# Performance work log

Hardware: AMD Instinct MI355X
Metric: run time of the kernel (lower is better)

## Reference

```python
import jax, jax.numpy as jnp
import numpy as np

N, E, H, L, R, NG = 8192, 131072, 256, 3, 128, 64
NUM_ELEMENTS = 80
CUTOFF = 12.0
INV_SQRT_2 = 1.0 / np.sqrt(2.0)
INV_SQRT_3 = 1.0 / np.sqrt(3.0)
INV_SQRT_H = 1.0 / np.sqrt(H)


def _glorot(key, shape):
    fan_in, fan_out = shape[-2], shape[-1]
    return jax.random.normal(key, shape, jnp.float32) * np.sqrt(2.0 / (fan_in + fan_out))


def setup_inputs():
    key = jax.random.key(0)
    ks = jax.random.split(key, 24)
    pos = jax.random.normal(ks[0], (N, 3), jnp.float32) * 5.0
    z = jax.random.randint(ks[1], (N,), 0, NUM_ELEMENTS)
    src = jax.random.randint(ks[2], (E,), 0, N)
    off = jax.random.randint(ks[3], (E,), 1, N)
    dst = (src + off) % N  # guarantee no self-loops (dist > 0)
    edge_index = jnp.stack([src, dst])
    batch = jnp.sort(jax.random.randint(ks[4], (N,), 0, NG))
    return {
        "pos": pos,
        "atom_emb": jax.random.normal(ks[5], (NUM_ELEMENTS, H), jnp.float32),
        "ln_w": jnp.ones((L, H), jnp.float32),
        "ln_b": jnp.zeros((L, H), jnp.float32),
        "xp_w1": _glorot(ks[6], (L, H, H)),
        "xp_b1": jnp.zeros((L, H), jnp.float32),
        "xp_w2": _glorot(ks[7], (L, H, 3 * H)),
        "xp_b2": jnp.zeros((L, 3 * H), jnp.float32),
        "rbf_w": _glorot(ks[8], (L, R, 3 * H)),
        "rbf_b": jnp.zeros((L, 3 * H), jnp.float32),
        "vec_w": _glorot(ks[9], (L, H, 2 * H)),
        "xv_w1": _glorot(ks[10], (L, 2 * H, H)),
        "xv_b1": jnp.zeros((L, H), jnp.float32),
        "xv_w2": _glorot(ks[11], (L, H, 3 * H)),
        "xv_b2": jnp.zeros((L, 3 * H), jnp.float32),
        "oe_w1": _glorot(ks[12], (H, H // 2)),
        "oe_b1": jnp.zeros((H // 2,), jnp.float32),
        "oe_w2": _glorot(ks[13], (H // 2, 1)),
        "oe_b2": jnp.zeros((1,), jnp.float32),
        "z": z,
        "edge_index": edge_index,
        "batch": batch,
    }


def _gaussian_rbf(dist):
    offset = jnp.linspace(0.0, CUTOFF, R)
    coeff = -0.5 / (offset[1] - offset[0]) ** 2
    return jnp.exp(coeff * (dist[:, None] - offset[None, :]) ** 2)  # [E, R]


def _layernorm(x, w, b):
    mu = x.mean(-1, keepdims=True)
    var = x.var(-1, keepdims=True)
    return (x - mu) / jnp.sqrt(var + 1e-5) * w + b


def reference(pos, atom_emb, ln_w, ln_b, xp_w1, xp_b1, xp_w2, xp_b2,
              rbf_w, rbf_b, vec_w, xv_w1, xv_b1, xv_w2, xv_b2,
              oe_w1, oe_b1, oe_w2, oe_b2, z, edge_index, batch):
    src, dst = edge_index[0], edge_index[1]
    rel = pos[src] - pos[dst]                       # [E, 3]
    dist = jnp.sqrt((rel ** 2).sum(-1))             # [E]
    edge_rbf = _gaussian_rbf(dist)                  # [E, R]
    edge_vector = rel / dist[:, None]               # [E, 3] unit vectors

    x = atom_emb[z]                                 # [N, H]
    vec = jnp.zeros((N, 3, H), x.dtype)

    for l in range(L):
        # ---- PaiNNMessage ----
        xh = _layernorm(x, ln_w[l], ln_b[l])
        xh = jax.nn.silu(xh @ xp_w1[l] + xp_b1[l]) @ xp_w2[l] + xp_b2[l]  # [N, 3H]
        rbfh = edge_rbf @ rbf_w[l] + rbf_b[l]                             # [E, 3H]
        m = xh[src] * rbfh
        mx, xh2, xh3 = jnp.split(m, 3, axis=-1)
        xh2 = xh2 * INV_SQRT_3
        mvec = (vec[src] * xh2[:, None, :] + xh3[:, None, :] * edge_vector[:, :, None]) * INV_SQRT_H
        dx = jax.ops.segment_sum(mx, dst, num_segments=N)
        dvec = jax.ops.segment_sum(mvec, dst, num_segments=N)
        x = (x + dx) * INV_SQRT_2
        vec = vec + dvec

        # ---- PaiNNUpdate ----
        vp = vec @ vec_w[l]                          # [N, 3, 2H]
        vec1, vec2 = jnp.split(vp, 2, axis=-1)
        vec_dot = (vec1 * vec2).sum(axis=1) * INV_SQRT_H           # [N, H]
        vnorm = jnp.sqrt((vec2 ** 2).sum(axis=1) + 1e-8)           # [N, H]
        h = jnp.concatenate([x, vnorm], axis=-1)
        h = jax.nn.silu(h @ xv_w1[l] + xv_b1[l]) @ xv_w2[l] + xv_b2[l]
        xv1, xv2, xv3 = jnp.split(h, 3, axis=-1)
        dx = (xv1 + xv2 * vec_dot) * INV_SQRT_2
        dvec = xv3[:, None, :] * vec1
        x = (x + dx) * INV_SQRT_2
        vec = vec + dvec

    # ---- energy head: per-atom MLP then per-molecule sum ----
    per_atom = jax.nn.silu(x @ oe_w1 + oe_b1) @ oe_w2 + oe_b2      # [N, 1]
    energy = jax.ops.segment_sum(per_atom, batch, num_segments=NG)  # [NG, 1]
    return energy
```

## Files before the change

### kernel.cpp

```cpp
#include <hip/hip_runtime.h>
#include <hip/hip_bf16.h>
#include <math.h>

#define NN 8192
#define EE 131072
#define HH 256
#define LL 3
#define RR 128
#define NGG 64
#define MSG_WAVES 16

typedef __attribute__((ext_vector_type(8))) short bf16x8;
typedef __attribute__((ext_vector_type(4))) float f32x4;
typedef unsigned short u16;

#if defined(__has_builtin)
#if __has_builtin(__builtin_amdgcn_fdot2_f32_bf16)
#define HAVE_FDOT2 1
typedef __attribute__((ext_vector_type(2))) __bf16 bf16x2_t;
union BU { unsigned u; bf16x2_t v; };
#endif
#if __has_builtin(__builtin_amdgcn_global_load_lds)
#define HAVE_GLL 1
#endif
#endif

union U4 { ushort4 v; unsigned short a[4]; };
union U8 { uint4 v; unsigned short a[8]; unsigned w[4]; };

__device__ __forceinline__ float silu(float v) { return v / (1.0f + expf(-v)); }
__device__ __forceinline__ float b2f(unsigned short u) { return __uint_as_float(((unsigned)u) << 16); }
__device__ __forceinline__ unsigned short f2b(float f) {
    unsigned u = __float_as_uint(f);
    u += 0x7fff + ((u >> 16) & 1);
    return (unsigned short)(u >> 16);
}

constexpr float kInvSqrt2 = 0.70710678118654752440f;
constexpr float kInvSqrt3 = 0.57735026918962576451f;
constexpr float kInvSqrtH = 0.0625f;

__global__ void k_zero(float* __restrict__ p, int n4) {
    int i = blockIdx.x * 256 + threadIdx.x;
    if (i < n4) ((float4*)p)[i] = make_float4(0.f, 0.f, 0.f, 0.f);
}

__global__ __launch_bounds__(256) void k_wt_all(
    const float* __restrict__ xp_w1, const float* __restrict__ xp_w2,
    const float* __restrict__ rbf_w, const float* __restrict__ vec_w,
    const float* __restrict__ xv_w1, const float* __restrict__ xv_w2,
    const float* __restrict__ oe_w1,
    u16* __restrict__ xp_w1T, u16* __restrict__ xp_w2T, u16* __restrict__ rbf_wP,
    u16* __restrict__ vec_wT, u16* __restrict__ xv_w1T, u16* __restrict__ xv_w2T,
    u16* __restrict__ oe_w1T) {
    int bid = blockIdx.x;
    const float* src; u16* dst; int K, N, t, pairmode = 0;
    if (bid < 2400) {
        int l = bid / 800, r = bid % 800;
        if (r < 64)       { src = xp_w1 + (size_t)l * 65536;  dst = xp_w1T + (size_t)l * 65536;  K = 256; N = 256; t = r; }
        else if (r < 256) { src = xp_w2 + (size_t)l * 196608; dst = xp_w2T + (size_t)l * 196608; K = 256; N = 768; t = r - 64; }
        else if (r < 352) { src = rbf_w + (size_t)l * 98304;  dst = rbf_wP + (size_t)l * 98304;  K = 128; N = 768; t = r - 256; pairmode = 1; }
        else if (r < 480) { src = vec_w + (size_t)l * 131072; dst = vec_wT + (size_t)l * 131072; K = 256; N = 512; t = r - 352; }
        else if (r < 608) { src = xv_w1 + (size_t)l * 131072; dst = xv_w1T + (size_t)l * 131072; K = 512; N = 256; t = r - 480; }
        else              { src = xv_w2 + (size_t)l * 196608; dst = xv_w2T + (size_t)l * 196608; K = 256; N = 768; t = r - 608; }
    } else {
        src = oe_w1; dst = oe_w1T; K = 256; N = 128; t = bid - 2400;
    }
    int nx = N >> 5;
    int bn = (t % nx) * 32, bk = (t / nx) * 32;
    int tx = threadIdx.x & 31, ty = threadIdx.x >> 5;
    if (pairmode) {
#pragma unroll
        for (int i = 0; i < 32; i += 8) {
            int k = bk + ty + i, n = bn + tx;
            dst[(size_t)(k >> 1) * 1536 + n * 2 + (k & 1)] = f2b(src[(size_t)k * N + n]);
        }
        return;
    }
    __shared__ float tile[32][33];
#pragma unroll
    for (int i = 0; i < 32; i += 8)
        tile[ty + i][tx] = src[(size_t)(bk + ty + i) * N + bn + tx];
    __syncthreads();
#pragma unroll
    for (int i = 0; i < 32; i += 8)
        dst[(size_t)(bn + ty + i) * K + bk + tx] = f2b(tile[tx][ty + i]);
}

__global__ void k_init_ln(const float* __restrict__ emb, const int* __restrict__ z,
                          const float* __restrict__ w, const float* __restrict__ b,
                          float* __restrict__ x, u16* __restrict__ xlnb) {
    int n = blockIdx.x, t = threadIdx.x;
    float v = emb[z[n] * HH + t];
    x[(size_t)n * HH + t] = v;
    float s = v, q = v * v;
#pragma unroll
    for (int m = 32; m >= 1; m >>= 1) {
        s += __shfl_xor(s, m, 64);
        q += __shfl_xor(q, m, 64);
    }
    __shared__ float s_sum[4], s_sq[4];
    int wid = t >> 6;
    if ((t & 63) == 0) { s_sum[wid] = s; s_sq[wid] = q; }
    __syncthreads();
    float S = s_sum[0] + s_sum[1] + s_sum[2] + s_sum[3];
    float Q = s_sq[0] + s_sq[1] + s_sq[2] + s_sq[3];
    float mu = S * (1.0f / HH);
    float var = Q * (1.0f / HH) - mu * mu;
    float rs = rsqrtf(var + 1e-5f);
    xlnb[(size_t)n * HH + t] = f2b((v - mu) * rs * w[t] + b[t]);
}

__global__ void k_geom_hist(const float* __restrict__ pos, const int* __restrict__ ei,
                            float* __restrict__ ev, int* __restrict__ deg) {
    int e = blockIdx.x * 256 + threadIdx.x;
    if (e >= EE) return;
    int s = ei[e], d = ei[EE + e];
    float rx = pos[s * 3 + 0] - pos[d * 3 + 0];
    float ry = pos[s * 3 + 1] - pos[d * 3 + 1];
    float rz = pos[s * 3 + 2] - pos[d * 3 + 2];
    float dist = sqrtf(rx * rx + ry * ry + rz * rz);
    float inv = 1.0f / dist;
    ((float4*)ev)[e] = make_float4(rx * inv, ry * inv, rz * inv, dist);
    atomicAdd(&deg[d], 1);
}

__global__ void k_scan_sort(const int* __restrict__ deg, int* __restrict__ row_ptr,
                            int* __restrict__ fill, int* __restrict__ dorder) {
    __shared__ int buf[256];
    __shared__ int carry_s;
    int t = threadIdx.x;
    if (t == 0) carry_s = 0;
    __syncthreads();
    for (int r = 0; r < NN; r += 256) {
        int v = deg[r + t];
        buf[t] = v;
        __syncthreads();
        for (int ofs = 1; ofs < 256; ofs <<= 1) {
            int add = (t >= ofs) ? buf[t - ofs] : 0;
            __syncthreads();
            buf[t] += add;
            __syncthreads();
        }
        int excl = buf[t] - v;
        int carry = carry_s;
        row_ptr[r + t] = carry + excl;
        fill[r + t] = carry + excl;
        __syncthreads();
        if (t == 255) carry_s = carry + buf[t];
        __syncthreads();
    }
    if (t == 0) row_ptr[NN] = carry_s;
    __syncthreads();
    __shared__ int bins[256];
    __shared__ int base[256];
    bins[t] = 0;
    __syncthreads();
    for (int d = t; d < NN; d += 256) {
        int b = deg[d]; b = b > 255 ? 255 : b;
        atomicAdd(&bins[b], 1);
    }
    __syncthreads();
    if (t == 0) {
        int acc = 0;
        for (int k = 255; k >= 0; --k) { base[k] = acc; acc += bins[k]; }
    }
    __syncthreads();
    bins[t] = 0;
    __syncthreads();
    for (int d = t; d < NN; d += 256) {
        int b = deg[d]; b = b > 255 ? 255 : b;
        int p = atomicAdd(&bins[b], 1);
        dorder[base[b] + p] = d;
    }
}

__global__ void k_scatter(const int* __restrict__ ei, const float* __restrict__ ev,
                          int* __restrict__ fill, int* __restrict__ srcp,
                          float4* __restrict__ evp, int* __restrict__ kptab,
                          unsigned* __restrict__ gtab) {
    int e = blockIdx.x * 256 + threadIdx.x;
    if (e >= EE) return;
    int d = ei[EE + e];
    int pos = atomicAdd(&fill[d], 1);
    float4 e4 = ((const float4*)ev)[e];
    srcp[pos] = ei[e];
    evp[pos] = e4;
    const float step = 12.0f / 127.0f;
    const float coeff = -0.5f / (step * step);
    float dist = e4.w;
    int k0 = ((int)floorf(dist / step) - 3) & ~1;
    k0 = k0 < 0 ? 0 : (k0 > 120 ? 120 : k0);
    float g[8];
#pragma unroll
    for (int k = 0; k < 8; ++k) {
        float t = dist - (k0 + k) * step;
        g[k] = expf(coeff * t * t);
    }
    kptab[pos] = k0 >> 1;
    unsigned g0 = (unsigned)f2b(g[0]) | ((unsigned)f2b(g[1]) << 16);
    unsigned g1 = (unsigned)f2b(g[2]) | ((unsigned)f2b(g[3]) << 16);
    unsigned g2 = (unsigned)f2b(g[4]) | ((unsigned)f2b(g[5]) << 16);
    unsigned g3 = (unsigned)f2b(g[6]) | ((unsigned)f2b(g[7]) << 16);
    ((uint4*)gtab)[pos] = make_uint4(g0, g1, g2, g3);
}

template <int OUT_BF16, int ACT>
__global__ __launch_bounds__(256) void k_gemm(
    const u16* __restrict__ A, const u16* __restrict__ BT,
    const float* __restrict__ bias, void* __restrict__ C, int M, int K, int N) {
    __shared__ u16 As[4096];
    __shared__ u16 Bs[4096];
    int tid = threadIdx.x;
    int wave = tid >> 6, lane = tid & 63;
    int bm = blockIdx.y * 128, bn = blockIdx.x * 128;
    int wm = (wave >> 1) * 64, wn = (wave & 1) * 64;
    int lm = lane & 15;
    int kg = lane >> 4;
    f32x4 acc[4][4] = {};

    for (int k0 = 0; k0 < K; k0 += 32) {
#pragma unroll
        for (int it = 0; it < 2; ++it) {
            int idx = it * 256 + tid;
            int r = idx >> 2, seg = idx & 3;
#ifdef HAVE_GLL
            __builtin_amdgcn_global_load_lds(
                (const unsigned*)&A[(size_t)(bm + r) * K + k0 + seg * 8],
                (unsigned*)&As[idx * 8], 16, 0, 0);
            __builtin_amdgcn_global_load_lds(
                (const unsigned*)&BT[(size_t)(bn + r) * K + k0 + seg * 8],
                (unsigned*)&Bs[idx * 8], 16, 0, 0);
#else
            *(uint4*)&As[idx * 8] = *(const uint4*)&A[(size_t)(bm + r) * K + k0 + seg * 8];
            *(uint4*)&Bs[idx * 8] = *(const uint4*)&BT[(size_t)(bn + r) * K + k0 + seg * 8];
#endif
        }
        __syncthreads();
        bf16x8 af[4], bfr[4];
#pragma unroll
        for (int i = 0; i < 4; ++i)
            af[i] = *(const bf16x8*)&As[(wm + i * 16 + lm) * 32 + kg * 8];
#pragma unroll
        for (int j = 0; j < 4; ++j)
            bfr[j] = *(const bf16x8*)&Bs[(wn + j * 16 + lm) * 32 + kg * 8];
#pragma unroll
        for (int i = 0; i < 4; ++i)
#pragma unroll
            for (int j = 0; j < 4; ++j)
                acc[i][j] = __builtin_amdgcn_mfma_f32_16x16x32_bf16(af[i], bfr[j], acc[i][j], 0, 0, 0);
        __syncthreads();
    }

#pragma unroll
    for (int j = 0; j < 4; ++j) {
        int col = bn + wn + j * 16 + lm;
        float bv = bias ? bias[col] : 0.f;
#pragma unroll
        for (int i = 0; i < 4; ++i) {
            int row0 = bm + wm + i * 16 + kg * 4;
#pragma unroll
            for (int r = 0; r < 4; ++r) {
                float v = acc[i][j][r] + bv;
                if (ACT) v = silu(v);
                if (OUT_BF16)
                    ((u16*)C)[(size_t)(row0 + r) * N + col] = f2b(v);
                else
                    ((float*)C)[(size_t)(row0 + r) * N + col] = v;
            }
        }
    }
}

__global__ __launch_bounds__(1024) void k_msg(
    const u16* __restrict__ xhb, const u16* __restrict__ vinb,
    const int* __restrict__ srcp, const float4* __restrict__ evp,
    const int* __restrict__ row_ptr, const int* __restrict__ kptab,
    const unsigned* __restrict__ gtab, const u16* __restrict__ WP ,
    const float* __restrict__ rbias, float* __restrict__ x,
    const float* __restrict__ vin, u16* __restrict__ vecMb,
    const int* __restrict__ dorder) {
    __shared__ u16 Wp[64 * 512];
    int tid = threadIdx.x;
    int wave = tid >> 6, lane = tid & 63;
    int c0 = lane * 4;
    int d = dorder[blockIdx.x * MSG_WAVES + wave];
    int E0 = row_ptr[d], E1 = row_ptr[d + 1];
    float accv[3][4] = {};

#pragma unroll
    for (int p = 0; p < 3; ++p) {
        __syncthreads();
#pragma unroll
        for (int it = 0; it < 4; ++it) {
            int idx = it * 1024 + tid;
            int r = idx >> 6;
            int c8 = (idx & 63) * 8;
            *(uint4*)&Wp[r * 512 + c8] =
                *(const uint4*)&WP[(size_t)r * 1536 + p * 512 + c8];
        }
        __syncthreads();
        float4 bb = ((const float4*)(rbias + p * 256))[lane];
        float bias4[4] = {bb.x, bb.y, bb.z, bb.w};
        float accx[4] = {};
        for (int j = E0; j < E1; ++j) {
            int s = srcp[j];
            int kp = kptab[j];
            uint4 gt = ((const uint4*)gtab)[j];
            unsigned gp[4] = {gt.x, gt.y, gt.z, gt.w};
            float rr[4] = {bias4[0], bias4[1], bias4[2], bias4[3]};
#pragma unroll
            for (int p2 = 0; p2 < 4; ++p2) {
                U8 w;
                w.v = *(const uint4*)&Wp[(kp + p2) * 512 + c0 * 2];
#ifdef HAVE_FDOT2
                BU gv; gv.u = gp[p2];
#pragma unroll
                for (int c = 0; c < 4; ++c) {
                    BU wv; wv.u = w.w[c];
                    rr[c] = __builtin_amdgcn_fdot2_f32_bf16(wv.v, gv.v, rr[c], false);
                }
#else
                float ge = b2f((u16)(gp[p2] & 0xffff));
                float go = b2f((u16)(gp[p2] >> 16));
#pragma unroll
                for (int c = 0; c < 4; ++c)
                    rr[c] += ge * b2f(w.a[2 * c]) + go * b2f(w.a[2 * c + 1]);
#endif
            }
            if (p == 0) {
                U4 X; X.v = *(const ushort4*)(xhb + (size_t)s * 768 + c0);
#pragma unroll
                for (int c = 0; c < 4; ++c) accx[c] += b2f(X.a[c]) * rr[c];
            } else if (p == 1) {
                U4 X, V0, V1, V2;
                X.v = *(const ushort4*)(xhb + (size_t)s * 768 + 256 + c0);
                V0.v = *(const ushort4*)(vinb + (size_t)s * 768 + c0);
                V1.v = *(const ushort4*)(vinb + (size_t)s * 768 + 256 + c0);
                V2.v = *(const ushort4*)(vinb + (size_t)s * 768 + 512 + c0);
#pragma unroll
                for (int c = 0; c < 4; ++c) {
                    float m1 = b2f(X.a[c]) * rr[c] * kInvSqrt3;
                    accv[0][c] += b2f(V0.a[c]) * m1;
                    accv[1][c] += b2f(V1.a[c]) * m1;
                    accv[2][c] += b2f(V2.a[c]) * m1;
                }
            } else {
                U4 X; X.v = *(const ushort4*)(xhb + (size_t)s * 768 + 512 + c0);
                float4 ev4 = evp[j];
#pragma unroll
                for (int c = 0; c < 4; ++c) {
                    float m2 = b2f(X.a[c]) * rr[c];
                    accv[0][c] += m2 * ev4.x;
                    accv[1][c] += m2 * ev4.y;
                    accv[2][c] += m2 * ev4.z;
                }
            }
        }
        if (p == 0) {
            size_t xi = (size_t)d * 256 + c0;
            float4 xv = *(const float4*)&x[xi];
            xv.x = (xv.x + accx[0]) * kInvSqrt2;
            xv.y = (xv.y + accx[1]) * kInvSqrt2;
            xv.z = (xv.z + accx[2]) * kInvSqrt2;
            xv.w = (xv.w + accx[3]) * kInvSqrt2;
            *(float4*)&x[xi] = xv;
        }
    }
#pragma unroll
    for (int k = 0; k < 3; ++k) {
        size_t idx = (size_t)d * 768 + k * 256 + c0;
        float4 vv = *(const float4*)&vin[idx];
        ushort4 u;
        u.x = f2b(vv.x + accv[k][0] * kInvSqrtH);
        u.y = f2b(vv.y + accv[k][1] * kInvSqrtH);
        u.z = f2b(vv.z + accv[k][2] * kInvSqrtH);
        u.w = f2b(vv.w + accv[k][3] * kInvSqrtH);
        *(ushort4*)&vecMb[idx] = u;
    }
}

__global__ void k_vecdot(const u16* __restrict__ vp, const float* __restrict__ x,
                         float* __restrict__ vec_dot, u16* __restrict__ hcat) {
    int i = blockIdx.x * 256 + threadIdx.x;
    int n = i >> 8, c = i & 255;
    const u16* p = vp + (size_t)n * 1536;
    float dsum = 0.f, qsum = 0.f;
#pragma unroll
    for (int k = 0; k < 3; ++k) {
        float v1 = b2f(p[k * 512 + c]);
        float v2 = b2f(p[k * 512 + 256 + c]);
        dsum += v1 * v2;
        qsum += v2 * v2;
    }
    vec_dot[i] = dsum * kInvSqrtH;
    hcat[(size_t)n * 512 + c] = f2b(x[i]);
    hcat[(size_t)n * 512 + 256 + c] = f2b(sqrtf(qsum + 1e-8f));
}

__global__ void k_update_out(const u16* __restrict__ hout, const float* __restrict__ vec_dot,
                             const u16* __restrict__ vp, float* __restrict__ x,
                             const u16* __restrict__ vecMb, float* __restrict__ vfin,
                             u16* __restrict__ vb,
                             const float* __restrict__ lnw, const float* __restrict__ lnb,
                             u16* __restrict__ xout) {
    int n = blockIdx.x, t = threadIdx.x;
    size_t i = (size_t)n * 256 + t;
    float xv1 = b2f(hout[(size_t)n * 768 + t]);
    float xv2 = b2f(hout[(size_t)n * 768 + 256 + t]);
    float xv3 = b2f(hout[(size_t)n * 768 + 512 + t]);
    float dxv = (xv1 + xv2 * vec_dot[i]) * kInvSqrt2;
    float nx = (x[i] + dxv) * kInvSqrt2;
    x[i] = nx;
#pragma unroll
    for (int k = 0; k < 3; ++k) {
        size_t idx = (size_t)n * 768 + k * 256 + t;
        float nv = b2f(vecMb[idx]) + xv3 * b2f(vp[(size_t)n * 1536 + k * 512 + t]);
        vfin[idx] = nv;
        vb[idx] = f2b(nv);
    }
    if (lnw) {
        float s = nx, q = nx * nx;
#pragma unroll
        for (int m = 32; m >= 1; m >>= 1) {
            s += __shfl_xor(s, m, 64);
            q += __shfl_xor(q, m, 64);
        }
        __shared__ float s_sum[4], s_sq[4];
        int wid = t >> 6;
        if ((t & 63) == 0) { s_sum[wid] = s; s_sq[wid] = q; }
        __syncthreads();
        float S = s_sum[0] + s_sum[1] + s_sum[2] + s_sum[3];
        float Q = s_sq[0] + s_sq[1] + s_sq[2] + s_sq[3];
        float mu = S * (1.0f / HH);
        float var = Q * (1.0f / HH) - mu * mu;
        float rs = rsqrtf(var + 1e-5f);
        xout[i] = f2b((nx - mu) * rs * lnw[t] + lnb[t]);
    } else {
        xout[i] = f2b(nx);
    }
}

__global__ void k_energy2(const float* __restrict__ h, const float* __restrict__ w2,
                          const float* __restrict__ b2, const int* __restrict__ batch,
                          float* __restrict__ out) {
    __shared__ float g[NGG];
    int t = threadIdx.x;
    if (t < NGG) g[t] = 0.f;
    __syncthreads();
    int a = blockIdx.x * 256 + t;
    const float4* hr = (const float4*)(h + (size_t)a * 128);
    const float4* w4 = (const float4*)w2;
    float acc = 0.f;
#pragma unroll 8
    for (int i = 0; i < 32; ++i) {
        float4 hv = hr[i], wv = w4[i];
        acc += hv.x * wv.x + hv.y * wv.y + hv.z * wv.z + hv.w * wv.w;
    }
    acc += b2[0];
    atomicAdd(&g[batch[a]], acc);
    __syncthreads();
    if (t < NGG && g[t] != 0.f) atomicAdd(&out[t], g[t]);
}

extern "C" void kernel_launch(void* const* d_in, const int* in_sizes, int n_in,
                              void* d_out, int out_size, void* d_ws, size_t ws_size,
                              hipStream_t stream) {
    const float* pos      = (const float*)d_in[0];
    const float* atom_emb = (const float*)d_in[1];
    const float* ln_w     = (const float*)d_in[2];
    const float* ln_b     = (const float*)d_in[3];
    const float* xp_w1    = (const float*)d_in[4];
    const float* xp_b1    = (const float*)d_in[5];
    const float* xp_w2    = (const float*)d_in[6];
    const float* xp_b2    = (const float*)d_in[7];
    const float* rbf_w    = (const float*)d_in[8];
    const float* rbf_b    = (const float*)d_in[9];
    const float* vec_w    = (const float*)d_in[10];
    const float* xv_w1    = (const float*)d_in[11];
    const float* xv_b1    = (const float*)d_in[12];
    const float* xv_w2    = (const float*)d_in[13];
    const float* xv_b2    = (const float*)d_in[14];
    const float* oe_w1    = (const float*)d_in[15];
    const float* oe_b1    = (const float*)d_in[16];
    const float* oe_w2    = (const float*)d_in[17];
    const float* oe_b2    = (const float*)d_in[18];
    const int*   z        = (const int*)d_in[19];
    const int*   ei       = (const int*)d_in[20];
    const int*   batch    = (const int*)d_in[21];
    float* out = (float*)d_out;

    char* ws = (char*)d_ws;
    size_t off = 0;
    auto alloc = [&](size_t b) {
        void* p = ws + off;
        off = (off + b + 255) & ~(size_t)255;
        return p;
    };
    float*    x      = (float*)alloc((size_t)NN * HH * 4);
    float*    vecA   = (float*)alloc((size_t)NN * 768 * 4);
    u16*      vb     = (u16*)alloc((size_t)NN * 768 * 2);
    u16*      vecMb  = (u16*)alloc((size_t)NN * 768 * 2);
    u16*      xlnb   = (u16*)alloc((size_t)NN * HH * 2);
    u16*      t1b    = (u16*)alloc((size_t)NN * HH * 2);
    u16*      xhb    = (u16*)alloc((size_t)NN * 768 * 2);
    float*    vdot   = (float*)alloc((size_t)NN * HH * 4);
    u16*      vpb    = (u16*)alloc((size_t)NN * 1536 * 2);
    u16*      houtb  = (u16*)alloc((size_t)NN * 768 * 2);
    float*    ev     = (float*)alloc((size_t)EE * 4 * 4);
    int*      deg    = (int*)alloc((size_t)NN * 4);
    int*      row_ptr= (int*)alloc((size_t)(NN + 1) * 4);
    int*      fill   = (int*)alloc((size_t)NN * 4);
    int*      dorder = (int*)alloc((size_t)NN * 4);
    int*      srcp   = (int*)alloc((size_t)EE * 4);
    float4*   evp    = (float4*)alloc((size_t)EE * 16);
    int*      kptab  = (int*)alloc((size_t)EE * 4);
    unsigned* gtab   = (unsigned*)alloc((size_t)EE * 16);
    u16* xp_w1T   = (u16*)alloc((size_t)3 * 256 * 256 * 2);
    u16* xp_w2T   = (u16*)alloc((size_t)3 * 768 * 256 * 2);
    u16* rbf_wP   = (u16*)alloc((size_t)3 * 128 * 768 * 2);
    u16* vec_wT   = (u16*)alloc((size_t)3 * 512 * 256 * 2);
    u16* xv_w1T   = (u16*)alloc((size_t)3 * 256 * 512 * 2);
    u16* xv_w2T   = (u16*)alloc((size_t)3 * 768 * 256 * 2);
    u16* oe_w1T   = (u16*)alloc((size_t)128 * 256 * 2);
    (void)ws_size;

    u16*   h1b   = t1b;
    u16*   hcatb = xhb;
    float* heng  = vdot;
    u16*   xb    = xlnb;

    k_wt_all<<<2432, 256, 0, stream>>>(xp_w1, xp_w2, rbf_w, vec_w, xv_w1, xv_w2, oe_w1,
                                       xp_w1T, xp_w2T, rbf_wP, vec_wT, xv_w1T, xv_w2T, oe_w1T);
    k_zero<<<(36 * 1024 * 1024 / 16 + 255) / 256, 256, 0, stream>>>(vecA, 36 * 1024 * 1024 / 16);
    k_zero<<<8, 256, 0, stream>>>((float*)deg, NN / 4);
    k_init_ln<<<NN, 256, 0, stream>>>(atom_emb, z, ln_w, ln_b, x, xlnb);
    k_geom_hist<<<EE / 256, 256, 0, stream>>>(pos, ei, ev, deg);
    k_scan_sort<<<1, 256, 0, stream>>>(deg, row_ptr, fill, dorder);
    k_scatter<<<EE / 256, 256, 0, stream>>>(ei, ev, fill, srcp, evp, kptab, gtab);

    for (int l = 0; l < LL; ++l) {
        k_gemm<1, 1><<<dim3(2, NN / 128), 256, 0, stream>>>(
            xlnb, xp_w1T + (size_t)l * 256 * 256, xp_b1 + l * HH, t1b, NN, 256, 256);
        k_gemm<1, 0><<<dim3(6, NN / 128), 256, 0, stream>>>(
            t1b, xp_w2T + (size_t)l * 768 * 256, xp_b2 + l * 768, xhb, NN, 256, 768);
        k_msg<<<NN / MSG_WAVES, 1024, 0, stream>>>(
            xhb, vb, srcp, evp, row_ptr, kptab, gtab,
            rbf_wP + (size_t)l * 128 * 768, rbf_b + l * 768, x, vecA, vecMb, dorder);

        k_gemm<1, 0><<<dim3(4, 3 * NN / 128), 256, 0, stream>>>(
            vecMb, vec_wT + (size_t)l * 512 * 256, nullptr, vpb, 3 * NN, 256, 512);
        k_vecdot<<<NN, 256, 0, stream>>>(vpb, x, vdot, hcatb);
        k_gemm<1, 1><<<dim3(2, NN / 128), 256, 0, stream>>>(
            hcatb, xv_w1T + (size_t)l * 256 * 512, xv_b1 + l * HH, h1b, NN, 512, 256);
        k_gemm<1, 0><<<dim3(6, NN / 128), 256, 0, stream>>>(
            h1b, xv_w2T + (size_t)l * 768 * 256, xv_b2 + l * 768, houtb, NN, 256, 768);
        bool last = (l == LL - 1);
        k_update_out<<<NN, 256, 0, stream>>>(
            houtb, vdot, vpb, x, vecMb, vecA, vb,
            last ? nullptr : ln_w + (l + 1) * HH,
            last ? nullptr : ln_b + (l + 1) * HH, xlnb);
    }

    k_gemm<0, 1><<<dim3(1, NN / 128), 256, 0, stream>>>(
        xb, oe_w1T, oe_b1, heng, NN, 256, 128);
    k_zero<<<1, 256, 0, stream>>>(out, NGG / 4);
    k_energy2<<<32, 256, 0, stream>>>(heng, oe_w2, oe_b2, batch, out);
}
```

Before: 785.0 us.

## Split message passing into fixed edge chunks with atomic segment flushes

The message kernel now gives each wave a fixed chunk of 16 destination-sorted edges instead of one destination node, which removes the degree-sorted ordering and the load imbalance from uneven degrees. Partial sums are flushed with float atomics into new accumulators whenever the destination changes. A separate epilogue kernel then applies the residual updates. The accumulators reuse the vpb buffer and are zeroed inside the update kernel. The cost is many more global atomics, an extra kernel launch, and more zeroing traffic, and each 1024-thread block still reloads the weight panel for only 256 edges.

```diff
diff --git a/kernel.cpp b/kernel.cpp
--- a/kernel.cpp
+++ b/kernel.cpp
@@ -9,6 +9,7 @@
 #define RR 128
 #define NGG 64
 #define MSG_WAVES 16
+#define CHUNK 16
 
 typedef __attribute__((ext_vector_type(8))) short bf16x8;
 typedef __attribute__((ext_vector_type(4))) float f32x4;
@@ -125,8 +126,7 @@
     atomicAdd(&deg[d], 1);
 }
 
-__global__ void k_scan_sort(const int* __restrict__ deg, int* __restrict__ row_ptr,
-                            int* __restrict__ fill, int* __restrict__ dorder) {
+__global__ void k_scan(const int* __restrict__ deg, int* __restrict__ fill) {
     __shared__ int buf[256];
     __shared__ int carry_s;
     int t = threadIdx.x;
@@ -144,47 +144,24 @@
         }
         int excl = buf[t] - v;
         int carry = carry_s;
-        row_ptr[r + t] = carry + excl;
         fill[r + t] = carry + excl;
         __syncthreads();
         if (t == 255) carry_s = carry + buf[t];
         __syncthreads();
-    }
-    if (t == 0) row_ptr[NN] = carry_s;
-    __syncthreads();
-    __shared__ int bins[256];
-    __shared__ int base[256];
-    bins[t] = 0;
-    __syncthreads();
-    for (int d = t; d < NN; d += 256) {
-        int b = deg[d]; b = b > 255 ? 255 : b;
-        atomicAdd(&bins[b], 1);
-    }
-    __syncthreads();
-    if (t == 0) {
-        int acc = 0;
-        for (int k = 255; k >= 0; --k) { base[k] = acc; acc += bins[k]; }
-    }
-    __syncthreads();
-    bins[t] = 0;
-    __syncthreads();
-    for (int d = t; d < NN; d += 256) {
-        int b = deg[d]; b = b > 255 ? 255 : b;
-        int p = atomicAdd(&bins[b], 1);
-        dorder[base[b] + p] = d;
     }
 }
 
 __global__ void k_scatter(const int* __restrict__ ei, const float* __restrict__ ev,
                           int* __restrict__ fill, int* __restrict__ srcp,
                           float4* __restrict__ evp, int* __restrict__ kptab,
-                          unsigned* __restrict__ gtab) {
+                          unsigned* __restrict__ gtab, int* __restrict__ dstp) {
     int e = blockIdx.x * 256 + threadIdx.x;
     if (e >= EE) return;
     int d = ei[EE + e];
     int pos = atomicAdd(&fill[d], 1);
     float4 e4 = ((const float4*)ev)[e];
     srcp[pos] = ei[e];
+    dstp[pos] = d;
     evp[pos] = e4;
     const float step = 12.0f / 127.0f;
     const float coeff = -0.5f / (step * step);
@@ -275,18 +252,16 @@
 __global__ __launch_bounds__(1024) void k_msg(
     const u16* __restrict__ xhb, const u16* __restrict__ vinb,
     const int* __restrict__ srcp, const float4* __restrict__ evp,
-    const int* __restrict__ row_ptr, const int* __restrict__ kptab,
+    const int* __restrict__ dstp, const int* __restrict__ kptab,
     const unsigned* __restrict__ gtab, const u16* __restrict__ WP ,
-    const float* __restrict__ rbias, float* __restrict__ x,
-    const float* __restrict__ vin, u16* __restrict__ vecMb,
-    const int* __restrict__ dorder) {
+    const float* __restrict__ rbias,
+    float* __restrict__ accX, float* __restrict__ accV) {
     __shared__ u16 Wp[64 * 512];
     int tid = threadIdx.x;
     int wave = tid >> 6, lane = tid & 63;
     int c0 = lane * 4;
-    int d = dorder[blockIdx.x * MSG_WAVES + wave];
-    int E0 = row_ptr[d], E1 = row_ptr[d + 1];
-    float accv[3][4] = {};
+    int E0 = (blockIdx.x * MSG_WAVES + wave) * CHUNK;
+    int E1 = E0 + CHUNK;
 
 #pragma unroll
     for (int p = 0; p < 3; ++p) {
@@ -302,8 +277,29 @@
         __syncthreads();
         float4 bb = ((const float4*)(rbias + p * 256))[lane];
         float bias4[4] = {bb.x, bb.y, bb.z, bb.w};
-        float accx[4] = {};
+        float acc[3][4] = {};
+        int dcur = dstp[E0];
+        auto flush = [&](int dn) {
+            if (p == 0) {
+                float* q = accX + (size_t)dn * 256 + c0;
+#pragma unroll
+                for (int c = 0; c < 4; ++c) atomicAdd(q + c, acc[0][c]);
+            } else {
+                float* q = accV + (size_t)dn * 768 + c0;
+#pragma unroll
+                for (int k = 0; k < 3; ++k)
+#pragma unroll
+                    for (int c = 0; c < 4; ++c) atomicAdd(q + k * 256 + c, acc[k][c]);
+            }
+#pragma unroll
+            for (int k = 0; k < 3; ++k)
+#pragma unroll
+                for (int c = 0; c < 4; ++c) acc[k][c] = 0.f;
+        };
+#pragma unroll 2
         for (int j = E0; j < E1; ++j) {
+            int d = dstp[j];
+            if (d != dcur) { flush(dcur); dcur = d; }
             int s = srcp[j];
             int kp = kptab[j];
             uint4 gt = ((const uint4*)gtab)[j];
@@ -331,7 +327,7 @@
             if (p == 0) {
                 U4 X; X.v = *(const ushort4*)(xhb + (size_t)s * 768 + c0);
 #pragma unroll
-                for (int c = 0; c < 4; ++c) accx[c] += b2f(X.a[c]) * rr[c];
+                for (int c = 0; c < 4; ++c) acc[0][c] += b2f(X.a[c]) * rr[c];
             } else if (p == 1) {
                 U4 X, V0, V1, V2;
                 X.v = *(const ushort4*)(xhb + (size_t)s * 768 + 256 + c0);
@@ -341,9 +337,9 @@
 #pragma unroll
                 for (int c = 0; c < 4; ++c) {
                     float m1 = b2f(X.a[c]) * rr[c] * kInvSqrt3;
-                    accv[0][c] += b2f(V0.a[c]) * m1;
-                    accv[1][c] += b2f(V1.a[c]) * m1;
-                    accv[2][c] += b2f(V2.a[c]) * m1;
+                    acc[0][c] += b2f(V0.a[c]) * m1;
+                    acc[1][c] += b2f(V1.a[c]) * m1;
+                    acc[2][c] += b2f(V2.a[c]) * m1;
                 }
             } else {
                 U4 X; X.v = *(const ushort4*)(xhb + (size_t)s * 768 + 512 + c0);
@@ -351,32 +347,39 @@
 #pragma unroll
                 for (int c = 0; c < 4; ++c) {
                     float m2 = b2f(X.a[c]) * rr[c];
-                    accv[0][c] += m2 * ev4.x;
-                    accv[1][c] += m2 * ev4.y;
-                    accv[2][c] += m2 * ev4.z;
+                    acc[0][c] += m2 * ev4.x;
+                    acc[1][c] += m2 * ev4.y;
+                    acc[2][c] += m2 * ev4.z;
                 }
             }
         }
-        if (p == 0) {
-            size_t xi = (size_t)d * 256 + c0;
-            float4 xv = *(const float4*)&x[xi];
-            xv.x = (xv.x + accx[0]) * kInvSqrt2;
-            xv.y = (xv.y + accx[1]) * kInvSqrt2;
-            xv.z = (xv.z + accx[2]) * kInvSqrt2;
-            xv.w = (xv.w + accx[3]) * kInvSqrt2;
-            *(float4*)&x[xi] = xv;
-        }
-    }
-#pragma unroll
-    for (int k = 0; k < 3; ++k) {
-        size_t idx = (size_t)d * 768 + k * 256 + c0;
-        float4 vv = *(const float4*)&vin[idx];
+        flush(dcur);
+    }
+}
+
+__global__ void k_msg_epi(const float* __restrict__ accX, const float* __restrict__ accV,
+                          float* __restrict__ x, const float* __restrict__ vin,
+                          u16* __restrict__ vecMb) {
+    int n = blockIdx.x, t = threadIdx.x;
+    if (t < 64) {
+        size_t i = (size_t)n * 64 + t;
+        float4 xv = ((float4*)x)[i];
+        float4 av = ((const float4*)accX)[i];
+        xv.x = (xv.x + av.x) * kInvSqrt2;
+        xv.y = (xv.y + av.y) * kInvSqrt2;
+        xv.z = (xv.z + av.z) * kInvSqrt2;
+        xv.w = (xv.w + av.w) * kInvSqrt2;
+        ((float4*)x)[i] = xv;
+    } else {
+        size_t i = (size_t)n * 192 + (t - 64);
+        float4 vv = ((const float4*)vin)[i];
+        float4 av = ((const float4*)accV)[i];
         ushort4 u;
-        u.x = f2b(vv.x + accv[k][0] * kInvSqrtH);
-        u.y = f2b(vv.y + accv[k][1] * kInvSqrtH);
-        u.z = f2b(vv.z + accv[k][2] * kInvSqrtH);
-        u.w = f2b(vv.w + accv[k][3] * kInvSqrtH);
-        *(ushort4*)&vecMb[idx] = u;
+        u.x = f2b(vv.x + av.x * kInvSqrtH);
+        u.y = f2b(vv.y + av.y * kInvSqrtH);
+        u.z = f2b(vv.z + av.z * kInvSqrtH);
+        u.w = f2b(vv.w + av.w * kInvSqrtH);
+        ((ushort4*)vecMb)[i] = u;
     }
 }
 
@@ -403,7 +406,8 @@
                              const u16* __restrict__ vecMb, float* __restrict__ vfin,
                              u16* __restrict__ vb,
                              const float* __restrict__ lnw, const float* __restrict__ lnb,
-                             u16* __restrict__ xout) {
+                             u16* __restrict__ xout,
+                             float* __restrict__ azX, float* __restrict__ azV) {
     int n = blockIdx.x, t = threadIdx.x;
     size_t i = (size_t)n * 256 + t;
     float xv1 = b2f(hout[(size_t)n * 768 + t]);
@@ -438,6 +442,12 @@
         xout[i] = f2b((nx - mu) * rs * lnw[t] + lnb[t]);
     } else {
         xout[i] = f2b(nx);
+    }
+    if (azV) {
+        __syncthreads();
+        azX[i] = 0.f;
+#pragma unroll
+        for (int k = 0; k < 3; ++k) azV[(size_t)n * 768 + k * 256 + t] = 0.f;
     }
 }
 
@@ -506,13 +516,13 @@
     u16*      xhb    = (u16*)alloc((size_t)NN * 768 * 2);
     float*    vdot   = (float*)alloc((size_t)NN * HH * 4);
     u16*      vpb    = (u16*)alloc((size_t)NN * 1536 * 2);
+    float*    accX   = (float*)alloc((size_t)NN * HH * 4);
     u16*      houtb  = (u16*)alloc((size_t)NN * 768 * 2);
     float*    ev     = (float*)alloc((size_t)EE * 4 * 4);
     int*      deg    = (int*)alloc((size_t)NN * 4);
-    int*      row_ptr= (int*)alloc((size_t)(NN + 1) * 4);
     int*      fill   = (int*)alloc((size_t)NN * 4);
-    int*      dorder = (int*)alloc((size_t)NN * 4);
     int*      srcp   = (int*)alloc((size_t)EE * 4);
+    int*      dstp   = (int*)alloc((size_t)EE * 4);
     float4*   evp    = (float4*)alloc((size_t)EE * 16);
     int*      kptab  = (int*)alloc((size_t)EE * 4);
     unsigned* gtab   = (unsigned*)alloc((size_t)EE * 16);
@@ -529,24 +539,27 @@
     u16*   hcatb = xhb;
     float* heng  = vdot;
     u16*   xb    = xlnb;
+    float* accV  = (float*)vpb;
 
     k_wt_all<<<2432, 256, 0, stream>>>(xp_w1, xp_w2, rbf_w, vec_w, xv_w1, xv_w2, oe_w1,
                                        xp_w1T, xp_w2T, rbf_wP, vec_wT, xv_w1T, xv_w2T, oe_w1T);
     k_zero<<<(36 * 1024 * 1024 / 16 + 255) / 256, 256, 0, stream>>>(vecA, 36 * 1024 * 1024 / 16);
+    k_zero<<<(32 * 1024 * 1024 / 16 + 255) / 256, 256, 0, stream>>>((float*)vpb, 32 * 1024 * 1024 / 16);
     k_zero<<<8, 256, 0, stream>>>((float*)deg, NN / 4);
     k_init_ln<<<NN, 256, 0, stream>>>(atom_emb, z, ln_w, ln_b, x, xlnb);
     k_geom_hist<<<EE / 256, 256, 0, stream>>>(pos, ei, ev, deg);
-    k_scan_sort<<<1, 256, 0, stream>>>(deg, row_ptr, fill, dorder);
-    k_scatter<<<EE / 256, 256, 0, stream>>>(ei, ev, fill, srcp, evp, kptab, gtab);
+    k_scan<<<1, 256, 0, stream>>>(deg, fill);
+    k_scatter<<<EE / 256, 256, 0, stream>>>(ei, ev, fill, srcp, evp, kptab, gtab, dstp);
 
     for (int l = 0; l < LL; ++l) {
         k_gemm<1, 1><<<dim3(2, NN / 128), 256, 0, stream>>>(
             xlnb, xp_w1T + (size_t)l * 256 * 256, xp_b1 + l * HH, t1b, NN, 256, 256);
         k_gemm<1, 0><<<dim3(6, NN / 128), 256, 0, stream>>>(
             t1b, xp_w2T + (size_t)l * 768 * 256, xp_b2 + l * 768, xhb, NN, 256, 768);
-        k_msg<<<NN / MSG_WAVES, 1024, 0, stream>>>(
-            xhb, vb, srcp, evp, row_ptr, kptab, gtab,
-            rbf_wP + (size_t)l * 128 * 768, rbf_b + l * 768, x, vecA, vecMb, dorder);
+        k_msg<<<EE / (CHUNK * MSG_WAVES), 1024, 0, stream>>>(
+            xhb, vb, srcp, evp, dstp, kptab, gtab,
+            rbf_wP + (size_t)l * 128 * 768, rbf_b + l * 768, accX, accV);
+        k_msg_epi<<<NN, 256, 0, stream>>>(accX, accV, x, vecA, vecMb);
 
         k_gemm<1, 0><<<dim3(4, 3 * NN / 128), 256, 0, stream>>>(
             vecMb, vec_wT + (size_t)l * 512 * 256, nullptr, vpb, 3 * NN, 256, 512);
@@ -559,7 +572,8 @@
         k_update_out<<<NN, 256, 0, stream>>>(
             houtb, vdot, vpb, x, vecMb, vecA, vb,
             last ? nullptr : ln_w + (l + 1) * HH,
-            last ? nullptr : ln_b + (l + 1) * HH, xlnb);
+            last ? nullptr : ln_b + (l + 1) * HH, xlnb,
+            last ? nullptr : accX, last ? nullptr : accV);
     }
 
     k_gemm<0, 1><<<dim3(1, NN / 128), 256, 0, stream>>>(
```

Result: slower. 1.661 ms (+111.6%).
